# Kernel optimization log

Hardware: AMD Instinct MI355X
Metric: run time of the kernel (lower is better)

## Reference

```python
import jax, jax.numpy as jnp
import numpy as np

B, S, H, NH = 16, 512, 768, 12
HD = H // NH


def setup_inputs() -> dict:
    key = jax.random.key(0)
    ks = jax.random.split(key, 8)
    w = 0.02
    return {
        "x": jax.random.normal(ks[0], (B, S, H), jnp.float32),
        "key_padding_mask": jnp.zeros((B, S), jnp.bool_),
        "in_proj_w": jax.random.normal(ks[1], (3 * H, H), jnp.float32) * w,
        "in_proj_b": jnp.zeros((3 * H,), jnp.float32),
        "out_proj_w": jax.random.normal(ks[2], (H, H), jnp.float32) * w,
        "out_proj_b": jnp.zeros((H,), jnp.float32),
        "w1": jax.random.normal(ks[3], (4 * H, H), jnp.float32) * w,
        "b1": jnp.zeros((4 * H,), jnp.float32),
        "w2": jax.random.normal(ks[4], (H, 4 * H), jnp.float32) * w,
        "b2": jnp.zeros((H,), jnp.float32),
        "ln1_g": jnp.ones((H,), jnp.float32),
        "ln1_b": jnp.zeros((H,), jnp.float32),
        "ln2_g": jnp.ones((H,), jnp.float32),
        "ln2_b": jnp.zeros((H,), jnp.float32),
    }


def _layernorm(x, g, b, eps=1e-5):
    m = jnp.mean(x, axis=-1, keepdims=True)
    v = jnp.var(x, axis=-1, keepdims=True)
    return (x - m) / jnp.sqrt(v + eps) * g + b


def reference(x, key_padding_mask, in_proj_w, in_proj_b, out_proj_w, out_proj_b,
              w1, b1, w2, b2, ln1_g, ln1_b, ln2_g, ln2_b):
    b, s, h = x.shape
    # --- nn.MultiheadAttention (batch_first, need_weights, per-head weights) ---
    qkv = x @ in_proj_w.T + in_proj_b                      # [B,S,3H]
    q, k, v = jnp.split(qkv, 3, axis=-1)
    q = q.reshape(b, s, NH, HD).transpose(0, 2, 1, 3)      # [B,NH,S,HD]
    k = k.reshape(b, s, NH, HD).transpose(0, 2, 1, 3)
    v = v.reshape(b, s, NH, HD).transpose(0, 2, 1, 3)
    scale = 1.0 / np.sqrt(HD).astype(np.float32)
    scores = jnp.einsum('bhqd,bhkd->bhqk', q * scale, k)   # [B,NH,S,S]
    scores = jnp.where(key_padding_mask[:, None, None, :], -jnp.inf, scores)
    attn_weights = jax.nn.softmax(scores, axis=-1)         # returned per-head
    attn_out = jnp.einsum('bhqk,bhkd->bhqd', attn_weights, v)
    attn_out = attn_out.transpose(0, 2, 1, 3).reshape(b, s, h)
    attn_out = attn_out @ out_proj_w.T + out_proj_b
    # --- residual + LN, FFN + residual + LN (dropout is identity in eval) ---
    x = _layernorm(x + attn_out, ln1_g, ln1_b)
    ffn = jax.nn.gelu(x @ w1.T + b1, approximate=False) @ w2.T + b2
    x = _layernorm(x + ffn, ln2_g, ln2_b)
    return x, attn_weights
```

## Files before the change

### kernel.cpp

```cpp
#include <hip/hip_runtime.h>
#include <hip/hip_bf16.h>
#include <math.h>

typedef __bf16 bf16;
typedef __attribute__((ext_vector_type(8))) __bf16 bf16x8;
typedef __attribute__((ext_vector_type(4))) __bf16 bf16x4;
typedef __attribute__((ext_vector_type(4))) float f32x4;

#define B_  16
#define S_  512
#define H_  768
#define NH_ 12
#define HD_ 64
#define A_  (B_*S_)

__device__ __forceinline__ void gload_lds16(const void* g, void* l) {
  __builtin_amdgcn_global_load_lds((const __attribute__((address_space(1))) void*)g,
                                   (__attribute__((address_space(3))) void*)l, 16, 0, 0);
}

template<int EPI, int BN_>
__global__ __launch_bounds__(512, 2) void k_gemm(
    const bf16* __restrict__ Amat, const bf16* __restrict__ Bt,
    const float* __restrict__ bias, const float* __restrict__ resF,
    const bf16* __restrict__ resB,
    float* __restrict__ outF, bf16* __restrict__ outB,
    bf16* __restrict__ outQ, bf16* __restrict__ outK, bf16* __restrict__ outVT,
    int M, int N, int K)
{
  constexpr int NFRAG  = BN_ / 64;
  constexpr int UNITS  = 2 + NFRAG;
  constexpr int SLOT_E = 8192 + BN_ * 64;
  constexpr int WN     = BN_ / 4;
  __shared__ __align__(16) bf16 LDS[3 * SLOT_E];
  const int tid = threadIdx.x;
  const int w = tid >> 6, l = tid & 63;
  const int lr = l & 15, hi = l >> 4;
  const int wm = w >> 2, wn = w & 3;

  const int nbx = N / BN_;
  const int cpx = gridDim.x >> 3;
  const int sw  = (blockIdx.x & 7) * cpx + (blockIdx.x >> 3);
  const int by = sw / nbx, bx = sw - by * nbx;
  const int row0 = by * 128, col0 = bx * BN_;
  const int NT = K / 64;

  auto stage = [&](int t, int u) {
    bf16* slot = LDS + (t % 3) * SLOT_E;
    if (u < 2) {
      const int fc = u*512 + tid;
      const int r = fc >> 3, s = fc & 7;
      const int gs = s ^ (r & 7);
      gload_lds16(Amat + (size_t)(row0 + r)*K + t*64 + gs*8,
                  slot + (size_t)fc*8 - (size_t)l*8);
    } else {
      const int fc = (u-2)*512 + tid;
      const int r = fc >> 3, s = fc & 7;
      const int gs = s ^ (r & 7);
      gload_lds16(Bt + (size_t)(col0 + r)*K + t*64 + gs*8,
                  slot + 8192 + (size_t)fc*8 - (size_t)l*8);
    }
  };

  f32x4 acc[4][NFRAG] = {};

#pragma unroll
  for (int u = 0; u < UNITS; ++u) stage(0, u);
#pragma unroll
  for (int u = 0; u < UNITS; ++u) stage(1, u);
  if constexpr (UNITS == 5) asm volatile("s_waitcnt vmcnt(5)" ::: "memory");
  else                      asm volatile("s_waitcnt vmcnt(6)" ::: "memory");
  __builtin_amdgcn_s_barrier();

  for (int t = 0; t < NT; ++t) {
    const bf16* slot = LDS + (t % 3) * SLOT_E;
    const bool pre = (t + 2 < NT);

    bf16x8 af[4], bfr[NFRAG];
#pragma unroll
    for (int m = 0; m < 4; ++m) {
      const int r = wm*64 + m*16 + lr;
      af[m] = *(const bf16x8*)(slot + r*64 + (hi ^ (r & 7))*8);
    }
#pragma unroll
    for (int n = 0; n < NFRAG; ++n) {
      const int r = wn*WN + n*16 + lr;
      bfr[n] = *(const bf16x8*)(slot + 8192 + r*64 + (hi ^ (r & 7))*8);
    }
    if (pre) {
      stage(t+2, 0); stage(t+2, 1); stage(t+2, 2);
      if constexpr (UNITS == 6) stage(t+2, 3);
    }
    __builtin_amdgcn_s_barrier();
    asm volatile("s_waitcnt lgkmcnt(0)" ::: "memory");
    __builtin_amdgcn_sched_barrier(0);
    __builtin_amdgcn_s_setprio(1);
#pragma unroll
    for (int m = 0; m < 4; ++m)
#pragma unroll
      for (int n = 0; n < NFRAG; ++n)
        acc[m][n] = __builtin_amdgcn_mfma_f32_16x16x32_bf16(af[m], bfr[n], acc[m][n], 0, 0, 0);
    __builtin_amdgcn_s_setprio(0);
    __builtin_amdgcn_s_barrier();

#pragma unroll
    for (int m = 0; m < 4; ++m) {
      const int r = wm*64 + m*16 + lr;
      af[m] = *(const bf16x8*)(slot + r*64 + ((4 + hi) ^ (r & 7))*8);
    }
#pragma unroll
    for (int n = 0; n < NFRAG; ++n) {
      const int r = wn*WN + n*16 + lr;
      bfr[n] = *(const bf16x8*)(slot + 8192 + r*64 + ((4 + hi) ^ (r & 7))*8);
    }
    if (pre) {
      if constexpr (UNITS == 5) { stage(t+2, 3); stage(t+2, 4); }
      else                      { stage(t+2, 4); stage(t+2, 5); }
    }
    __builtin_amdgcn_s_barrier();
    asm volatile("s_waitcnt lgkmcnt(0)" ::: "memory");
    __builtin_amdgcn_sched_barrier(0);
    __builtin_amdgcn_s_setprio(1);
#pragma unroll
    for (int m = 0; m < 4; ++m)
#pragma unroll
      for (int n = 0; n < NFRAG; ++n)
        acc[m][n] = __builtin_amdgcn_mfma_f32_16x16x32_bf16(af[m], bfr[n], acc[m][n], 0, 0, 0);
    __builtin_amdgcn_s_setprio(0);

    if (t < NT - 1) {
      if (pre) {
        if constexpr (UNITS == 5) asm volatile("s_waitcnt vmcnt(5)" ::: "memory");
        else                      asm volatile("s_waitcnt vmcnt(6)" ::: "memory");
      } else {
        asm volatile("s_waitcnt vmcnt(0)" ::: "memory");
      }
      __builtin_amdgcn_s_barrier();
    }
  }

#pragma unroll
  for (int m = 0; m < 4; ++m) {
#pragma unroll
    for (int n = 0; n < NFRAG; ++n) {
#pragma unroll
      for (int i = 0; i < 4; ++i) {
        const int row = row0 + wm*64 + m*16 + hi*4 + i;
        const int col = col0 + wn*WN + n*16 + lr;
        float v = acc[m][n][i] + bias[col];
        if constexpr (EPI == 1) {
          v += resF[(size_t)row*N + col];
          outF[(size_t)row*N + col] = v;
        } else if constexpr (EPI == 2) {
          v = 0.5f * v * (1.0f + erff(v * 0.7071067811865475f));
          outB[(size_t)row*N + col] = (bf16)v;
        } else if constexpr (EPI == 3) {
          v += (float)resB[(size_t)row*N + col];
          outF[(size_t)row*N + col] = v;
        } else {
          const int b = row >> 9, s = row & 511;
          const int which = col / H_;
          const int hcol = col - which * H_;
          const int h = hcol >> 6, d = hcol & 63;
          const size_t bh = (size_t)b * NH_ + h;
          if (which == 0)      outQ[(bh*S_ + s)*HD_ + d] = (bf16)v;
          else if (which == 1) outK[(bh*S_ + s)*HD_ + d] = (bf16)v;
          else                 outVT[(bh*HD_ + d)*S_ + s] = (bf16)v;
        }
      }
    }
  }
}

__global__ __launch_bounds__(256) void k_attn_fused(
    const bf16* __restrict__ Qm, const bf16* __restrict__ Km, const bf16* __restrict__ VT,
    const unsigned char* __restrict__ mask, float* __restrict__ P, bf16* __restrict__ AO)
{
  __shared__ __align__(16) bf16 KVs[512*64];
  __shared__ __align__(16) bf16 Qs[64*64];
  const int tid = threadIdx.x, w = tid >> 6, l = tid & 63;
  const int lr = l & 15, hi = l >> 4;
  const int cpx = gridDim.x >> 3;
  const int sw  = (blockIdx.x & 7) * cpx + (blockIdx.x >> 3);
  const int bh = sw >> 3, qt = sw & 7;
  const int b = bh / NH_, h = bh - b * NH_;
  const int swz = (lr & 7) << 4;

  const bf16* Kg = Km + (size_t)bh * S_ * HD_;
  const bf16* Qg = Qm + (size_t)bh * S_ * HD_ + (size_t)qt * 64 * HD_;
#pragma unroll
  for (int rnd = 0; rnd < 16; ++rnd) {
    const int c = rnd*256 + tid;
    const int row = c >> 3, col16 = (c & 7) ^ (row & 7);
    gload_lds16(Kg + row*HD_ + col16*8, KVs + (rnd*4 + w)*512);
  }
#pragma unroll
  for (int rnd = 0; rnd < 2; ++rnd) {
    const int c = rnd*256 + tid;
    const int row = c >> 3, col16 = (c & 7) ^ (row & 7);
    gload_lds16(Qg + row*HD_ + col16*8, Qs + (rnd*4 + w)*512);
  }
  __syncthreads();

  const char* qrow = (const char*)(Qs + (w*16 + lr)*64);
  bf16x8 qf0 = *(const bf16x8*)(qrow + ((hi*16) ^ swz));
  bf16x8 qf1 = *(const bf16x8*)(qrow + ((64 + hi*16) ^ swz));
  f32x4 acc[32];
#pragma unroll
  for (int ct = 0; ct < 32; ++ct) acc[ct] = f32x4{0.f,0.f,0.f,0.f};
#pragma unroll
  for (int ct = 0; ct < 32; ++ct) {
    const char* kb = (const char*)(KVs + (ct*16 + lr)*64);
    bf16x8 a0 = *(const bf16x8*)(kb + ((hi*16) ^ swz));
    bf16x8 a1 = *(const bf16x8*)(kb + ((64 + hi*16) ^ swz));
    acc[ct] = __builtin_amdgcn_mfma_f32_16x16x32_bf16(a0, qf0, acc[ct], 0, 0, 0);
    acc[ct] = __builtin_amdgcn_mfma_f32_16x16x32_bf16(a1, qf1, acc[ct], 0, 0, 0);
  }
  __syncthreads();

  const bf16* Vg = VT + (size_t)bh * HD_ * S_;
#pragma unroll
  for (int rnd = 0; rnd < 16; ++rnd) {
    const int c = rnd*256 + tid;
    const int row = c >> 6, col16 = (c & 63) ^ (row & 7);
    gload_lds16(Vg + row*S_ + col16*8, KVs + (rnd*4 + w)*512);
  }

  const unsigned char* mrow = mask + b * S_;
  float mx = -1e30f;
#pragma unroll
  for (int ct = 0; ct < 32; ++ct) {
    const unsigned mk4 = *(const unsigned*)(mrow + ct*16 + hi*4);
#pragma unroll
    for (int i = 0; i < 4; ++i) {
      float v = acc[ct][i] * 0.125f;
      if ((mk4 >> (8*i)) & 0xff) v = -1e30f;
      acc[ct][i] = v;
      mx = fmaxf(mx, v);
    }
  }
  mx = fmaxf(mx, __shfl_xor(mx, 16));
  mx = fmaxf(mx, __shfl_xor(mx, 32));
  float sum = 0.f;
#pragma unroll
  for (int ct = 0; ct < 32; ++ct)
#pragma unroll
    for (int i = 0; i < 4; ++i) { float e = __expf(acc[ct][i] - mx); acc[ct][i] = e; sum += e; }
  sum += __shfl_xor(sum, 16);
  sum += __shfl_xor(sum, 32);
  const float inv = 1.f / sum;

  float* prow = P + ((size_t)bh*S_ + (size_t)qt*64 + w*16 + lr) * S_;
#pragma unroll
  for (int ct = 0; ct < 32; ++ct) {
#pragma unroll
    for (int i = 0; i < 4; ++i) acc[ct][i] *= inv;
    *(f32x4*)(prow + ct*16 + hi*4) = acc[ct];
  }
  __syncthreads();

  f32x4 o[4] = {};
#pragma unroll
  for (int c = 0; c < 16; ++c) {
    bf16x8 pa;
#pragma unroll
    for (int i = 0; i < 4; ++i) { pa[i] = (bf16)acc[2*c][i]; pa[4+i] = (bf16)acc[2*c+1][i]; }
    const int cb0 = (64*c + 8*hi) ^ swz;
    const int cb1 = (64*c + 32 + 8*hi) ^ swz;
#pragma unroll
    for (int nt = 0; nt < 4; ++nt) {
      const char* vb = (const char*)(KVs + (nt*16 + lr)*512);
      bf16x4 v0 = *(const bf16x4*)(vb + cb0);
      bf16x4 v1 = *(const bf16x4*)(vb + cb1);
      bf16x8 vf = {v0[0],v0[1],v0[2],v0[3], v1[0],v1[1],v1[2],v1[3]};
      o[nt] = __builtin_amdgcn_mfma_f32_16x16x32_bf16(pa, vf, o[nt], 0, 0, 0);
    }
  }

  bf16* aorow = AO + ((size_t)(b*S_ + qt*64 + w*16))*H_ + h*HD_;
#pragma unroll
  for (int nt = 0; nt < 4; ++nt)
#pragma unroll
    for (int i = 0; i < 4; ++i)
      aorow[(size_t)(hi*4 + i)*H_ + nt*16 + lr] = (bf16)o[nt][i];
}

__global__ __launch_bounds__(256) void k_layernorm(
    const float* __restrict__ X, const float* __restrict__ g, const float* __restrict__ bta,
    float* __restrict__ outF, bf16* __restrict__ outB)
{
  const int w = threadIdx.x >> 6, l = threadIdx.x & 63;
  const int row = blockIdx.x * 4 + w;
  const float* x = X + (size_t)row * H_;
  float4 v[3]; float s = 0.f, ss = 0.f;
#pragma unroll
  for (int j = 0; j < 3; ++j) {
    v[j] = *(const float4*)(x + l*4 + j*256);
    s  += v[j].x + v[j].y + v[j].z + v[j].w;
    ss += v[j].x*v[j].x + v[j].y*v[j].y + v[j].z*v[j].z + v[j].w*v[j].w;
  }
#pragma unroll
  for (int d = 1; d < 64; d <<= 1) { s += __shfl_xor(s, d); ss += __shfl_xor(ss, d); }
  const float mean = s * (1.f / H_);
  const float var  = ss * (1.f / H_) - mean * mean;
  const float inv  = rsqrtf(var + 1e-5f);
#pragma unroll
  for (int j = 0; j < 3; ++j) {
    const int c = l*4 + j*256;
    const float4 gv = *(const float4*)(g + c);
    const float4 bv = *(const float4*)(bta + c);
    float4 y;
    y.x = (v[j].x - mean)*inv*gv.x + bv.x;
    y.y = (v[j].y - mean)*inv*gv.y + bv.y;
    y.z = (v[j].z - mean)*inv*gv.z + bv.z;
    y.w = (v[j].w - mean)*inv*gv.w + bv.w;
    if (outF) *(float4*)(outF + (size_t)row*H_ + c) = y;
    if (outB) {
      bf16x4 o; o[0]=(bf16)y.x; o[1]=(bf16)y.y; o[2]=(bf16)y.z; o[3]=(bf16)y.w;
      *(bf16x4*)(outB + (size_t)row*H_ + c) = o;
    }
  }
}

#define NB0 (A_*H_/1024)
#define NB1 (3*H_*H_/1024)
#define NB2 (H_*H_/1024)
#define NB3 (4*H_*H_/1024)
#define NB4 (4*H_*H_/1024)
__global__ void k_conv_all(
    const float* __restrict__ s0, bf16* __restrict__ d0,
    const float* __restrict__ s1, bf16* __restrict__ d1,
    const float* __restrict__ s2, bf16* __restrict__ d2,
    const float* __restrict__ s3, bf16* __restrict__ d3,
    const float* __restrict__ s4, bf16* __restrict__ d4)
{
  int b = blockIdx.x;
  const float* src; bf16* dst;
  if      (b < NB0)                   { src = s0; dst = d0; }
  else if ((b -= NB0) < NB1)          { src = s1; dst = d1; }
  else if ((b -= NB1) < NB2)          { src = s2; dst = d2; }
  else if ((b -= NB2) < NB3)          { src = s3; dst = d3; }
  else    { b -= NB3;                   src = s4; dst = d4; }
  const int i = (b * 256 + threadIdx.x) * 4;
  const float4 vv = *(const float4*)(src + i);
  bf16x4 o; o[0]=(bf16)vv.x; o[1]=(bf16)vv.y; o[2]=(bf16)vv.z; o[3]=(bf16)vv.w;
  *(bf16x4*)(dst + i) = o;
}

extern "C" void kernel_launch(void* const* d_in, const int* in_sizes, int n_in,
                              void* d_out, int out_size, void* d_ws, size_t ws_size,
                              hipStream_t stream) {
  const float* x      = (const float*)d_in[0];
  const unsigned char* mask = (const unsigned char*)d_in[1];
  const float* w_qkv  = (const float*)d_in[2];
  const float* b_qkv  = (const float*)d_in[3];
  const float* w_out  = (const float*)d_in[4];
  const float* b_out  = (const float*)d_in[5];
  const float* w1     = (const float*)d_in[6];
  const float* b1     = (const float*)d_in[7];
  const float* w2     = (const float*)d_in[8];
  const float* b2     = (const float*)d_in[9];
  const float* ln1g   = (const float*)d_in[10];
  const float* ln1b   = (const float*)d_in[11];
  const float* ln2g   = (const float*)d_in[12];
  const float* ln2b   = (const float*)d_in[13];

  float* xout = (float*)d_out;
  float* P    = xout + (size_t)A_ * H_;

  char* ws = (char*)d_ws;
  size_t off = 0;
  auto alloc = [&](size_t bytes) { char* p = ws + off; off += (bytes + 255) & ~255ull; return p; };

  bf16* xb   = (bf16*)alloc((size_t)A_*H_*2);
  bf16* wqkv = (bf16*)alloc((size_t)3*H_*H_*2);
  bf16* wo   = (bf16*)alloc((size_t)H_*H_*2);
  bf16* w1b  = (bf16*)alloc((size_t)4*H_*H_*2);
  bf16* w2b  = (bf16*)alloc((size_t)4*H_*H_*2);
  char* qreg = alloc((size_t)A_*H_*2*4);
  bf16* q  = (bf16*)qreg;
  bf16* kb = q  + (size_t)A_*H_;
  bf16* vt = kb + (size_t)A_*H_;
  bf16* ao = vt + (size_t)A_*H_;
  bf16* hbuf = q;
  float* y1  = (float*)alloc((size_t)A_*H_*4);
  bf16*  x1b = (bf16*)alloc((size_t)A_*H_*2);

  k_conv_all<<<NB0+NB1+NB2+NB3+NB4, 256, 0, stream>>>(
      x, xb, w_qkv, wqkv, w_out, wo, w1, w1b, w2, w2b);

  k_gemm<0,192><<<(A_/128)*(3*H_/192), 512, 0, stream>>>(xb, wqkv, b_qkv, nullptr, nullptr,
      nullptr, nullptr, q, kb, vt, A_, 3*H_, H_);
  k_attn_fused<<<B_*NH_*8, 256, 0, stream>>>(q, kb, vt, mask, P, ao);
  k_gemm<1,192><<<(A_/128)*(H_/192), 512, 0, stream>>>(ao, wo, b_out, x, nullptr,
      y1, nullptr, nullptr, nullptr, nullptr, A_, H_, H_);
  k_layernorm<<<A_/4, 256, 0, stream>>>(y1, ln1g, ln1b, nullptr, x1b);
  k_gemm<2,256><<<(A_/128)*(4*H_/256), 512, 0, stream>>>(x1b, w1b, b1, nullptr, nullptr,
      nullptr, hbuf, nullptr, nullptr, nullptr, A_, 4*H_, H_);
  k_gemm<3,192><<<(A_/128)*(H_/192), 512, 0, stream>>>(hbuf, w2b, b2, nullptr, x1b,
      y1, nullptr, nullptr, nullptr, nullptr, A_, H_, 4*H_);
  k_layernorm<<<A_/4, 256, 0, stream>>>(y1, ln2g, ln2b, xout, nullptr);
}
```

Before: 313.8 us.

## Load GEMM A-operand directly to registers and store residual intermediates in bf16

```diff
diff --git a/kernel.cpp b/kernel.cpp
--- a/kernel.cpp
+++ b/kernel.cpp
@@ -22,15 +22,13 @@
 template<int EPI, int BN_>
 __global__ __launch_bounds__(512, 2) void k_gemm(
     const bf16* __restrict__ Amat, const bf16* __restrict__ Bt,
-    const float* __restrict__ bias, const float* __restrict__ resF,
-    const bf16* __restrict__ resB,
+    const float* __restrict__ bias, const bf16* __restrict__ resB,
     float* __restrict__ outF, bf16* __restrict__ outB,
     bf16* __restrict__ outQ, bf16* __restrict__ outK, bf16* __restrict__ outVT,
     int M, int N, int K)
 {
   constexpr int NFRAG  = BN_ / 64;
-  constexpr int UNITS  = 2 + NFRAG;
-  constexpr int SLOT_E = 8192 + BN_ * 64;
+  constexpr int SLOT_E = BN_ * 64;
   constexpr int WN     = BN_ / 4;
   __shared__ __align__(16) bf16 LDS[3 * SLOT_E];
   const int tid = threadIdx.x;
@@ -45,53 +43,47 @@
   const int row0 = by * 128, col0 = bx * BN_;
   const int NT = K / 64;
 
-  auto stage = [&](int t, int u) {
+  auto stageB = [&](int t, int u) {
     bf16* slot = LDS + (t % 3) * SLOT_E;
-    if (u < 2) {
-      const int fc = u*512 + tid;
-      const int r = fc >> 3, s = fc & 7;
-      const int gs = s ^ (r & 7);
-      gload_lds16(Amat + (size_t)(row0 + r)*K + t*64 + gs*8,
-                  slot + (size_t)fc*8 - (size_t)l*8);
-    } else {
-      const int fc = (u-2)*512 + tid;
-      const int r = fc >> 3, s = fc & 7;
-      const int gs = s ^ (r & 7);
-      gload_lds16(Bt + (size_t)(col0 + r)*K + t*64 + gs*8,
-                  slot + 8192 + (size_t)fc*8 - (size_t)l*8);
-    }
+    const int fc = u*512 + tid;
+    const int r = fc >> 3, s = fc & 7;
+    const int gs = s ^ (r & 7);
+    gload_lds16(Bt + (size_t)(col0 + r)*K + t*64 + gs*8,
+                slot + (size_t)fc*8 - (size_t)l*8);
   };
-
-  f32x4 acc[4][NFRAG] = {};
-
-#pragma unroll
-  for (int u = 0; u < UNITS; ++u) stage(0, u);
-#pragma unroll
-  for (int u = 0; u < UNITS; ++u) stage(1, u);
-  if constexpr (UNITS == 5) asm volatile("s_waitcnt vmcnt(5)" ::: "memory");
-  else                      asm volatile("s_waitcnt vmcnt(6)" ::: "memory");
-  __builtin_amdgcn_s_barrier();
-
-  for (int t = 0; t < NT; ++t) {
-    const bf16* slot = LDS + (t % 3) * SLOT_E;
-    const bool pre = (t + 2 < NT);
-
-    bf16x8 af[4], bfr[NFRAG];
+  const bf16* arow = Amat + (size_t)(row0 + wm*64 + lr) * K + hi*8;
+  auto loadA = [&](int t, bf16x8 (&fr)[8]) {
 #pragma unroll
     for (int m = 0; m < 4; ++m) {
-      const int r = wm*64 + m*16 + lr;
-      af[m] = *(const bf16x8*)(slot + r*64 + (hi ^ (r & 7))*8);
-    }
+      fr[m]     = *(const bf16x8*)(arow + (size_t)m*16*K + t*64);
+      fr[4 + m] = *(const bf16x8*)(arow + (size_t)m*16*K + t*64 + 32);
+    }
+  };
+  auto ldsReadB = [&](const bf16* slot, int ks, bf16x8 (&bf)[NFRAG]) {
 #pragma unroll
     for (int n = 0; n < NFRAG; ++n) {
       const int r = wn*WN + n*16 + lr;
-      bfr[n] = *(const bf16x8*)(slot + 8192 + r*64 + (hi ^ (r & 7))*8);
-    }
-    if (pre) {
-      stage(t+2, 0); stage(t+2, 1); stage(t+2, 2);
-      if constexpr (UNITS == 6) stage(t+2, 3);
-    }
-    __builtin_amdgcn_s_barrier();
+      bf[n] = *(const bf16x8*)(slot + r*64 + ((ks*4 + hi) ^ (r & 7))*8);
+    }
+  };
+
+  f32x4 acc[4][NFRAG] = {};
+  bf16x8 aP[8], aQ[8];
+
+#pragma unroll
+  for (int u = 0; u < NFRAG; ++u) stageB(0, u);
+  loadA(0, aP);
+#pragma unroll
+  for (int u = 0; u < NFRAG; ++u) stageB(1, u);
+  if constexpr (NFRAG == 3) asm volatile("s_waitcnt vmcnt(3)" ::: "memory");
+  else                      asm volatile("s_waitcnt vmcnt(4)" ::: "memory");
+  __builtin_amdgcn_s_barrier();
+
+  auto gemm_tile = [&](int t, bf16x8 (&aCur)[8], bf16x8 (&aNext)[8]) {
+    const bf16* slot = LDS + (t % 3) * SLOT_E;
+    bf16x8 bf0[NFRAG];
+    ldsReadB(slot, 0, bf0);
+    if (t + 1 < NT) loadA(t + 1, aNext);
     asm volatile("s_waitcnt lgkmcnt(0)" ::: "memory");
     __builtin_amdgcn_sched_barrier(0);
     __builtin_amdgcn_s_setprio(1);
@@ -99,25 +91,14 @@
     for (int m = 0; m < 4; ++m)
 #pragma unroll
       for (int n = 0; n < NFRAG; ++n)
-        acc[m][n] = __builtin_amdgcn_mfma_f32_16x16x32_bf16(af[m], bfr[n], acc[m][n], 0, 0, 0);
+        acc[m][n] = __builtin_amdgcn_mfma_f32_16x16x32_bf16(aCur[m], bf0[n], acc[m][n], 0, 0, 0);
     __builtin_amdgcn_s_setprio(0);
-    __builtin_amdgcn_s_barrier();
-
-#pragma unroll
-    for (int m = 0; m < 4; ++m) {
-      const int r = wm*64 + m*16 + lr;
-      af[m] = *(const bf16x8*)(slot + r*64 + ((4 + hi) ^ (r & 7))*8);
-    }
-#pragma unroll
-    for (int n = 0; n < NFRAG; ++n) {
-      const int r = wn*WN + n*16 + lr;
-      bfr[n] = *(const bf16x8*)(slot + 8192 + r*64 + ((4 + hi) ^ (r & 7))*8);
-    }
-    if (pre) {
-      if constexpr (UNITS == 5) { stage(t+2, 3); stage(t+2, 4); }
-      else                      { stage(t+2, 4); stage(t+2, 5); }
-    }
-    __builtin_amdgcn_s_barrier();
+    bf16x8 bf1[NFRAG];
+    ldsReadB(slot, 1, bf1);
+    if (t + 2 < NT) {
+#pragma unroll
+      for (int u = 0; u < NFRAG; ++u) stageB(t + 2, u);
+    }
     asm volatile("s_waitcnt lgkmcnt(0)" ::: "memory");
     __builtin_amdgcn_sched_barrier(0);
     __builtin_amdgcn_s_setprio(1);
@@ -125,18 +106,22 @@
     for (int m = 0; m < 4; ++m)
 #pragma unroll
       for (int n = 0; n < NFRAG; ++n)
-        acc[m][n] = __builtin_amdgcn_mfma_f32_16x16x32_bf16(af[m], bfr[n], acc[m][n], 0, 0, 0);
+        acc[m][n] = __builtin_amdgcn_mfma_f32_16x16x32_bf16(aCur[4 + m], bf1[n], acc[m][n], 0, 0, 0);
     __builtin_amdgcn_s_setprio(0);
-
     if (t < NT - 1) {
-      if (pre) {
-        if constexpr (UNITS == 5) asm volatile("s_waitcnt vmcnt(5)" ::: "memory");
-        else                      asm volatile("s_waitcnt vmcnt(6)" ::: "memory");
+      if (t + 2 < NT) {
+        if constexpr (NFRAG == 3) asm volatile("s_waitcnt vmcnt(3)" ::: "memory");
+        else                      asm volatile("s_waitcnt vmcnt(4)" ::: "memory");
       } else {
         asm volatile("s_waitcnt vmcnt(0)" ::: "memory");
       }
       __builtin_amdgcn_s_barrier();
     }
+  };
+
+  for (int tt = 0; tt < NT; tt += 2) {
+    gemm_tile(tt,     aP, aQ);
+    gemm_tile(tt + 1, aQ, aP);
   }
 
 #pragma unroll
@@ -148,15 +133,12 @@
         const int row = row0 + wm*64 + m*16 + hi*4 + i;
         const int col = col0 + wn*WN + n*16 + lr;
         float v = acc[m][n][i] + bias[col];
-        if constexpr (EPI == 1) {
-          v += resF[(size_t)row*N + col];
-          outF[(size_t)row*N + col] = v;
-        } else if constexpr (EPI == 2) {
+        if constexpr (EPI == 2) {
           v = 0.5f * v * (1.0f + erff(v * 0.7071067811865475f));
           outB[(size_t)row*N + col] = (bf16)v;
-        } else if constexpr (EPI == 3) {
+        } else if constexpr (EPI == 4) {
           v += (float)resB[(size_t)row*N + col];
-          outF[(size_t)row*N + col] = v;
+          outB[(size_t)row*N + col] = (bf16)v;
         } else {
           const int b = row >> 9, s = row & 511;
           const int which = col / H_;
@@ -177,7 +159,6 @@
     const unsigned char* __restrict__ mask, float* __restrict__ P, bf16* __restrict__ AO)
 {
   __shared__ __align__(16) bf16 KVs[512*64];
-  __shared__ __align__(16) bf16 Qs[64*64];
   const int tid = threadIdx.x, w = tid >> 6, l = tid & 63;
   const int lr = l & 15, hi = l >> 4;
   const int cpx = gridDim.x >> 3;
@@ -187,24 +168,17 @@
   const int swz = (lr & 7) << 4;
 
   const bf16* Kg = Km + (size_t)bh * S_ * HD_;
-  const bf16* Qg = Qm + (size_t)bh * S_ * HD_ + (size_t)qt * 64 * HD_;
 #pragma unroll
   for (int rnd = 0; rnd < 16; ++rnd) {
     const int c = rnd*256 + tid;
     const int row = c >> 3, col16 = (c & 7) ^ (row & 7);
     gload_lds16(Kg + row*HD_ + col16*8, KVs + (rnd*4 + w)*512);
   }
-#pragma unroll
-  for (int rnd = 0; rnd < 2; ++rnd) {
-    const int c = rnd*256 + tid;
-    const int row = c >> 3, col16 = (c & 7) ^ (row & 7);
-    gload_lds16(Qg + row*HD_ + col16*8, Qs + (rnd*4 + w)*512);
-  }
+  const bf16* qrow_g = Qm + (size_t)bh * S_ * HD_ + (size_t)(qt*64 + w*16 + lr) * HD_;
+  bf16x8 qf0 = *(const bf16x8*)(qrow_g + hi*8);
+  bf16x8 qf1 = *(const bf16x8*)(qrow_g + 32 + hi*8);
   __syncthreads();
 
-  const char* qrow = (const char*)(Qs + (w*16 + lr)*64);
-  bf16x8 qf0 = *(const bf16x8*)(qrow + ((hi*16) ^ swz));
-  bf16x8 qf1 = *(const bf16x8*)(qrow + ((64 + hi*16) ^ swz));
   f32x4 acc[32];
 #pragma unroll
   for (int ct = 0; ct < 32; ++ct) acc[ct] = f32x4{0.f,0.f,0.f,0.f};
@@ -286,18 +260,21 @@
 }
 
 __global__ __launch_bounds__(256) void k_layernorm(
-    const float* __restrict__ X, const float* __restrict__ g, const float* __restrict__ bta,
+    const bf16* __restrict__ X, const float* __restrict__ g, const float* __restrict__ bta,
     float* __restrict__ outF, bf16* __restrict__ outB)
 {
   const int w = threadIdx.x >> 6, l = threadIdx.x & 63;
   const int row = blockIdx.x * 4 + w;
-  const float* x = X + (size_t)row * H_;
-  float4 v[3]; float s = 0.f, ss = 0.f;
+  const bf16* x = X + (size_t)row * H_;
+  float v[12]; float s = 0.f, ss = 0.f;
 #pragma unroll
   for (int j = 0; j < 3; ++j) {
-    v[j] = *(const float4*)(x + l*4 + j*256);
-    s  += v[j].x + v[j].y + v[j].z + v[j].w;
-    ss += v[j].x*v[j].x + v[j].y*v[j].y + v[j].z*v[j].z + v[j].w*v[j].w;
+    bf16x4 b4 = *(const bf16x4*)(x + l*4 + j*256);
+#pragma unroll
+    for (int e = 0; e < 4; ++e) {
+      const float f = (float)b4[e];
+      v[j*4 + e] = f; s += f; ss += f*f;
+    }
   }
 #pragma unroll
   for (int d = 1; d < 64; d <<= 1) { s += __shfl_xor(s, d); ss += __shfl_xor(ss, d); }
@@ -310,10 +287,10 @@
     const float4 gv = *(const float4*)(g + c);
     const float4 bv = *(const float4*)(bta + c);
     float4 y;
-    y.x = (v[j].x - mean)*inv*gv.x + bv.x;
-    y.y = (v[j].y - mean)*inv*gv.y + bv.y;
-    y.z = (v[j].z - mean)*inv*gv.z + bv.z;
-    y.w = (v[j].w - mean)*inv*gv.w + bv.w;
+    y.x = (v[j*4+0] - mean)*inv*gv.x + bv.x;
+    y.y = (v[j*4+1] - mean)*inv*gv.y + bv.y;
+    y.z = (v[j*4+2] - mean)*inv*gv.z + bv.z;
+    y.w = (v[j*4+3] - mean)*inv*gv.w + bv.w;
     if (outF) *(float4*)(outF + (size_t)row*H_ + c) = y;
     if (outB) {
       bf16x4 o; o[0]=(bf16)y.x; o[1]=(bf16)y.y; o[2]=(bf16)y.z; o[3]=(bf16)y.w;
@@ -383,21 +360,22 @@
   bf16* vt = kb + (size_t)A_*H_;
   bf16* ao = vt + (size_t)A_*H_;
   bf16* hbuf = q;
-  float* y1  = (float*)alloc((size_t)A_*H_*4);
-  bf16*  x1b = (bf16*)alloc((size_t)A_*H_*2);
+  bf16* y1b = (bf16*)alloc((size_t)A_*H_*2);
+  bf16* y2b = (bf16*)alloc((size_t)A_*H_*2);
+  bf16* x1b = (bf16*)alloc((size_t)A_*H_*2);
 
   k_conv_all<<<NB0+NB1+NB2+NB3+NB4, 256, 0, stream>>>(
       x, xb, w_qkv, wqkv, w_out, wo, w1, w1b, w2, w2b);
 
-  k_gemm<0,192><<<(A_/128)*(3*H_/192), 512, 0, stream>>>(xb, wqkv, b_qkv, nullptr, nullptr,
+  k_gemm<0,192><<<(A_/128)*(3*H_/192), 512, 0, stream>>>(xb, wqkv, b_qkv, nullptr,
       nullptr, nullptr, q, kb, vt, A_, 3*H_, H_);
   k_attn_fused<<<B_*NH_*8, 256, 0, stream>>>(q, kb, vt, mask, P, ao);
-  k_gemm<1,192><<<(A_/128)*(H_/192), 512, 0, stream>>>(ao, wo, b_out, x, nullptr,
-      y1, nullptr, nullptr, nullptr, nullptr, A_, H_, H_);
-  k_layernorm<<<A_/4, 256, 0, stream>>>(y1, ln1g, ln1b, nullptr, x1b);
-  k_gemm<2,256><<<(A_/128)*(4*H_/256), 512, 0, stream>>>(x1b, w1b, b1, nullptr, nullptr,
+  k_gemm<4,192><<<(A_/128)*(H_/192), 512, 0, stream>>>(ao, wo, b_out, xb,
+      nullptr, y1b, nullptr, nullptr, nullptr, A_, H_, H_);
+  k_layernorm<<<A_/4, 256, 0, stream>>>(y1b, ln1g, ln1b, nullptr, x1b);
+  k_gemm<2,256><<<(A_/128)*(4*H_/256), 512, 0, stream>>>(x1b, w1b, b1, nullptr,
       nullptr, hbuf, nullptr, nullptr, nullptr, A_, 4*H_, H_);
-  k_gemm<3,192><<<(A_/128)*(H_/192), 512, 0, stream>>>(hbuf, w2b, b2, nullptr, x1b,
-      y1, nullptr, nullptr, nullptr, nullptr, A_, H_, 4*H_);
-  k_layernorm<<<A_/4, 256, 0, stream>>>(y1, ln2g, ln2b, xout, nullptr);
-}
+  k_gemm<4,192><<<(A_/128)*(H_/192), 512, 0, stream>>>(hbuf, w2b, b2, x1b,
+      nullptr, y2b, nullptr, nullptr, nullptr, A_, H_, 4*H_);
+  k_layernorm<<<A_/4, 256, 0, stream>>>(y2b, ln2g, ln2b, xout, nullptr);
+}
```

After: 486.6 us. +55.1%, slower.
